# Performance work log

Measured on AMD Instinct MI355X. Metric: run time of the kernel, lower is better.

## Reference

```python
import jax, jax.numpy as jnp
import numpy as np

TAU = 2.0        # tau_m
EPS = 1e-5       # BatchNorm eps
SG_GAIN = 4.0    # surrogate gradient gain for LIF nodes
GATE_GAIN = 10.0 # SCALPerceptionLayer gain
GATE_VTH = 0.5   # SCALPerceptionLayer v_th_init


def _spike(v, v_th, gain):
    # Heaviside forward, sigmoid surrogate backward (straight-through).
    s = jax.nn.sigmoid(gain * (v - v_th))
    hard = (v >= v_th).astype(v.dtype)
    return s + jax.lax.stop_gradient(hard - s)


def _lif(x, v_th):
    # single-step LIF, zero initial membrane: v = v0 + (x - v0)/tau = x/tau
    return _spike(x / TAU, v_th, SG_GAIN)


def _bn(x, gamma, beta):
    # BatchNorm1d over channel dim D of (B, N, D): stats over (B, N)
    m = x.mean(axis=(0, 1))
    v = x.var(axis=(0, 1))
    return (x - m) * jax.lax.rsqrt(v + EPS) * gamma + beta


def setup_inputs() -> dict:
    B, N, D, H = 4, 1024, 1024, 16
    key = jax.random.key(0)
    ks = jax.random.split(key, 12)
    def lin(k, out_f, in_f):
        return jax.random.normal(k, (out_f, in_f), jnp.float32) * (in_f ** -0.5)
    inp = {"x": jax.random.normal(ks[0], (B, N, D), jnp.float32)}
    for i, nm in enumerate(["q", "k", "v", "p"]):
        inp[f"W{nm}"] = lin(ks[1 + i], D, D)
        inp[f"b{nm}"] = jnp.zeros((D,), jnp.float32)
        inp[f"g{nm}"] = jnp.ones((D,), jnp.float32)   # BN gamma
        inp[f"beta{nm}"] = jnp.zeros((D,), jnp.float32)  # BN beta
    inp["Wg"] = lin(ks[10], H, D)  # logic_core linear
    inp["bg"] = jnp.zeros((H,), jnp.float32)
    return inp


def reference(x, Wq, bq, gq, betaq, Wk, bk, gk, betak,
              Wv, bv, gv, betav, Wp, bp, gp, betap, Wg, bg):
    B, N, D = x.shape
    H = Wg.shape[0]
    hd = D // H
    scale = hd ** -0.125

    def branch(W, b, g, beta):
        # Linear -> BN (over channels) -> LIF spike -> (B,H,N,hd)
        s = _lif(_bn(x @ W.T + b, g, beta), 1.0)
        return s.reshape(B, N, H, hd).transpose(0, 2, 1, 3)

    q = branch(Wq, bq, gq, betaq)
    k = branch(Wk, bk, gk, betak)
    v = branch(Wv, bv, gv, betav)

    # LogicGateController: energy (B,H) -> repeat to (B,D) -> spiking linear gate
    energy = (q * k).sum(axis=-1).mean(axis=-1)            # (B, H)
    energy_feat = jnp.tile(energy, (1, D // H))            # (B, D)
    gate = _spike(energy_feat @ Wg.T + bg, GATE_VTH, GATE_GAIN)  # (B, H)
    gate = gate[:, :, None, None]                          # (B, H, 1, 1)

    attn = jnp.einsum('bhnd,bhmd->bhnm', q, k) * scale     # (B,H,N,N)
    x_attn = jnp.einsum('bhnm,bhmd->bhnd', attn * gate, v) # (B,H,N,hd)
    x_attn = x_attn.transpose(0, 2, 1, 3).reshape(B, N, D)
    x_attn = _lif(x_attn, 0.5)                             # attn_lif, v_th=0.5

    out = _lif(_bn(x_attn @ Wp.T + bp, gp, betap), 1.0)    # proj path
    return out
```

## Files before the change

kernel.cpp:

```cpp
#include <hip/hip_runtime.h>
#include <cstddef>
#include <cstdint>

#define EPS 1e-5f

typedef __bf16 bf16x8 __attribute__((ext_vector_type(8)));
typedef float f32x4 __attribute__((ext_vector_type(4)));
typedef unsigned short u16x8 __attribute__((ext_vector_type(8)));

__device__ __forceinline__ unsigned short f2bf(float f) {
  unsigned u = __builtin_bit_cast(unsigned, f);
  unsigned r = u + 0x7FFFu + ((u >> 16) & 1u);
  return (unsigned short)(r >> 16);
}
__device__ __forceinline__ float bf2f(unsigned short h) {
  unsigned u = (unsigned)h << 16;
  return __builtin_bit_cast(float, u);
}

__device__ __forceinline__ void gl_lds16(const void* g, void* l) {
  __builtin_amdgcn_global_load_lds(
      (const __attribute__((address_space(1))) unsigned int*)g,
      (__attribute__((address_space(3))) unsigned int*)l, 16, 0, 0);
}

template <int MODE>
__global__ __launch_bounds__(256) void gemm_bf16_bt(
    const unsigned short* __restrict__ A,
    const unsigned short* __restrict__ W0, const unsigned short* __restrict__ W1,
    const float* __restrict__ b0, const float* __restrict__ b1,
    unsigned short* __restrict__ Y, double* __restrict__ psum, double* __restrict__ psq,
    const int* __restrict__ flags, int N, int Kc)
{
  if (MODE == 2) { if (flags[0] == 0) return; }

  __shared__ unsigned short As[2][8192];
  __shared__ unsigned short Bs[2][8192];
  const int tid = threadIdx.x;

  const int bid = blockIdx.x + (blockIdx.y << 3) + (blockIdx.z << 8);
  const int nwg = (int)gridDim.z << 8;
  const int cpx = nwg >> 3;
  const int sw = (bid & 7) * cpx + (bid >> 3);
  const int bx = sw & 7, by = (sw >> 3) & 31, z = sw >> 8;

  const unsigned short* Bm = z ? W1 : W0;
  const float* bias = z ? b1 : b0;
  unsigned short* Yz = Y + (size_t)z * 4096 * N;

  const int bm = by * 128, bn = bx * 128;
  const int lane = tid & 63, w = tid >> 6;
  const int wr = w >> 1, wc = w & 1;
  const int l15 = lane & 15, g = lane >> 4;

  f32x4 acc[4][4] = {};

  bool skip = false;
  if (MODE == 1) skip = (flags[1 + (by >> 3)] == 0);

  if (!skip) {
    const unsigned short* aSrc[4]; const unsigned short* bSrc[4]; int dOff[4];
#pragma unroll
    for (int c = 0; c < 4; ++c) {
      int S = c * 256 + tid;
      int row = S >> 3, sp = S & 7;
      int sl = sp ^ (row & 7);
      aSrc[c] = A  + (size_t)(bm + row) * Kc + sl * 8;
      bSrc[c] = Bm + (size_t)(bn + row) * Kc + sl * 8;
      dOff[c] = S * 8;
    }
    int aOff[4][2], bOff[4][2];
#pragma unroll
    for (int i = 0; i < 4; ++i)
#pragma unroll
      for (int t = 0; t < 2; ++t) {
        int rowA = wr * 64 + i * 16 + l15;
        aOff[i][t] = rowA * 64 + ((t * 4 + g) ^ (rowA & 7)) * 8;
        int rowB = wc * 64 + i * 16 + l15;
        bOff[i][t] = rowB * 64 + ((t * 4 + g) ^ (rowB & 7)) * 8;
      }

    const int nk = Kc >> 6;
#pragma unroll
    for (int c = 0; c < 4; ++c) { gl_lds16(aSrc[c], &As[0][dOff[c]]); aSrc[c] += 64; }
#pragma unroll
    for (int c = 0; c < 4; ++c) { gl_lds16(bSrc[c], &Bs[0][dOff[c]]); bSrc[c] += 64; }

    int cur = 0;
    for (int kt = 0; kt < nk; ++kt) {
      if (kt + 1 < nk) {
#pragma unroll
        for (int c = 0; c < 4; ++c) { gl_lds16(aSrc[c], &As[cur ^ 1][dOff[c]]); aSrc[c] += 64; }
#pragma unroll
        for (int c = 0; c < 4; ++c) { gl_lds16(bSrc[c], &Bs[cur ^ 1][dOff[c]]); bSrc[c] += 64; }
        asm volatile("s_waitcnt vmcnt(8)" ::: "memory");
      } else {
        asm volatile("s_waitcnt vmcnt(0)" ::: "memory");
      }
      __builtin_amdgcn_s_barrier();
      __builtin_amdgcn_sched_barrier(0);
      {
        const unsigned short* Ac = &As[cur][0];
        const unsigned short* Bc = &Bs[cur][0];
#pragma unroll
        for (int t = 0; t < 2; ++t) {
          bf16x8 af[4], bfr[4];
#pragma unroll
          for (int i = 0; i < 4; ++i) af[i] = *(const bf16x8*)&Ac[aOff[i][t]];
#pragma unroll
          for (int j = 0; j < 4; ++j) bfr[j] = *(const bf16x8*)&Bc[bOff[j][t]];
#pragma unroll
          for (int i = 0; i < 4; ++i)
#pragma unroll
            for (int j = 0; j < 4; ++j)
              acc[i][j] = __builtin_amdgcn_mfma_f32_16x16x32_bf16(af[i], bfr[j], acc[i][j], 0, 0, 0);
        }
      }
      __builtin_amdgcn_s_barrier();
      cur ^= 1;
    }
  }

  const int r0 = bm + wr * 64 + g * 4;
  float csum[4], csq[4];
#pragma unroll
  for (int j = 0; j < 4; ++j) { csum[j] = 0.f; csq[j] = 0.f; }
#pragma unroll
  for (int j = 0; j < 4; ++j) {
    int col = bn + wc * 64 + j * 16 + l15;
    float bv = bias[col];
#pragma unroll
    for (int i = 0; i < 4; ++i)
#pragma unroll
      for (int r = 0; r < 4; ++r) {
        float yv = acc[i][j][r] + bv;
        unsigned short h = f2bf(yv);
        float yb = bf2f(h);
        Yz[(size_t)(r0 + i * 16 + r) * N + col] = h;
        csum[j] += yb;
        csq[j] += yb * yb;
      }
  }
  __syncthreads();
  float* Ls = (float*)&As[0][0];
  const int slot = wr * 4 + g;
#pragma unroll
  for (int j = 0; j < 4; ++j) {
    int ci = wc * 64 + j * 16 + l15;
    Ls[slot * 128 + ci] = csum[j];
    Ls[1024 + slot * 128 + ci] = csq[j];
  }
  __syncthreads();
  if (tid < 128) {
    double s = 0.0, q = 0.0;
#pragma unroll
    for (int sl = 0; sl < 8; ++sl) {
      s += (double)Ls[sl * 128 + tid];
      q += (double)Ls[1024 + sl * 128 + tid];
    }
    size_t o = ((size_t)z * 32 + by) * N + bn + tid;
    psum[o] = s;
    psq[o] = q;
  }
}

__global__ void prep1_kernel(const float* __restrict__ x,
                             const float* __restrict__ Wq, const float* __restrict__ Wk,
                             unsigned short* __restrict__ Xh, unsigned short* __restrict__ Wh3)
{
  int bid = blockIdx.x, tid = threadIdx.x;
  const float* src; unsigned short* dst; size_t base;
  if (bid < 2048) {
    src = x; dst = Xh; base = ((size_t)bid * 256 + tid) * 8;
  } else if (bid < 2560) {
    src = Wq; dst = Wh3; base = ((size_t)(bid - 2048) * 256 + tid) * 8;
  } else {
    src = Wk; dst = Wh3 + (size_t)1024 * 1024; base = ((size_t)(bid - 2560) * 256 + tid) * 8;
  }
  float4 a = *reinterpret_cast<const float4*>(&src[base]);
  float4 b = *reinterpret_cast<const float4*>(&src[base + 4]);
  u16x8 o;
  o[0] = f2bf(a.x); o[1] = f2bf(a.y); o[2] = f2bf(a.z); o[3] = f2bf(a.w);
  o[4] = f2bf(b.x); o[5] = f2bf(b.y); o[6] = f2bf(b.z); o[7] = f2bf(b.w);
  *reinterpret_cast<u16x8*>(&dst[base]) = o;
}

__global__ void prep2_kernel(const float* __restrict__ Wv, const float* __restrict__ Wp,
                             unsigned short* __restrict__ Whv, unsigned short* __restrict__ Wpcat,
                             const int* __restrict__ flags)
{
  if (flags[0] == 0) return;
  int bid = blockIdx.x, tid = threadIdx.x;
  if (bid < 512) {
    size_t base = ((size_t)bid * 256 + tid) * 8;
    float4 a = *reinterpret_cast<const float4*>(&Wv[base]);
    float4 b = *reinterpret_cast<const float4*>(&Wv[base + 4]);
    u16x8 o;
    o[0] = f2bf(a.x); o[1] = f2bf(a.y); o[2] = f2bf(a.z); o[3] = f2bf(a.w);
    o[4] = f2bf(b.x); o[5] = f2bf(b.y); o[6] = f2bf(b.z); o[7] = f2bf(b.w);
    *reinterpret_cast<u16x8*>(&Whv[base]) = o;
  } else {
    size_t base = ((size_t)(bid - 512) * 256 + tid) * 8;
    int r = (int)(base >> 10), c = (int)(base & 1023);
    float4 a = *reinterpret_cast<const float4*>(&Wp[base]);
    float4 b = *reinterpret_cast<const float4*>(&Wp[base + 4]);
    u16x8 hi, lo;
    hi[0] = f2bf(a.x); lo[0] = f2bf(a.x - bf2f(hi[0]));
    hi[1] = f2bf(a.y); lo[1] = f2bf(a.y - bf2f(hi[1]));
    hi[2] = f2bf(a.z); lo[2] = f2bf(a.z - bf2f(hi[2]));
    hi[3] = f2bf(a.w); lo[3] = f2bf(a.w - bf2f(hi[3]));
    hi[4] = f2bf(b.x); lo[4] = f2bf(b.x - bf2f(hi[4]));
    hi[5] = f2bf(b.y); lo[5] = f2bf(b.y - bf2f(hi[5]));
    hi[6] = f2bf(b.z); lo[6] = f2bf(b.z - bf2f(hi[6]));
    hi[7] = f2bf(b.w); lo[7] = f2bf(b.w - bf2f(hi[7]));
    unsigned short* Or = Wpcat + (size_t)r * 2048;
    *reinterpret_cast<u16x8*>(&Or[c]) = hi;
    *reinterpret_cast<u16x8*>(&Or[1024 + c]) = lo;
  }
}

__global__ void bn_finalize(const double* __restrict__ psum, const double* __restrict__ psq,
                            const float* __restrict__ g0, const float* __restrict__ g1,
                            float* __restrict__ meanv, float* __restrict__ Av,
                            const int* __restrict__ runflag,
                            int* __restrict__ zflags, int* __restrict__ zenergy,
                            int N, double invM)
{
  if (zflags && blockIdx.x == 0 && blockIdx.y == 0) {
    int t = threadIdx.x;
    if (t < 5) zflags[t] = 0;
    if (t >= 64 && t < 128) zenergy[t - 64] = 0;
  }
  if (runflag && runflag[0] == 0) return;
  int z = blockIdx.y;
  const float* g = z ? g1 : g0;
  int c = blockIdx.x * blockDim.x + threadIdx.x;
  const double* ps = psum + (size_t)z * 32 * N + c;
  const double* pq = psq  + (size_t)z * 32 * N + c;
  double s0 = 0, s1 = 0, q0 = 0, q1 = 0;
#pragma unroll
  for (int rb = 0; rb < 32; rb += 2) {
    s0 += ps[(size_t)rb * N];       q0 += pq[(size_t)rb * N];
    s1 += ps[(size_t)(rb + 1) * N]; q1 += pq[(size_t)(rb + 1) * N];
  }
  double s = s0 + s1, q = q0 + q1;
  double m = s * invM;
  double var = q * invM - m * m;
  if (var < 0.0) var = 0.0;
  meanv[(size_t)z * N + c] = (float)m;
  Av[(size_t)z * N + c] = g[(size_t)c] * rsqrtf((float)var + EPS);
}

__global__ void spike_qk_energy(const unsigned short* __restrict__ Yq,
                                const unsigned short* __restrict__ Yk,
                                const float* __restrict__ meanv, const float* __restrict__ Av,
                                const float* __restrict__ beq, const float* __restrict__ bek,
                                unsigned short* __restrict__ qb, unsigned short* __restrict__ kb,
                                int* __restrict__ energy_int, int N)
{
  const int tid = threadIdx.x;
  const int c0 = (tid * 8) & (N - 1);
  const int head = c0 >> 6;
  const int batch = blockIdx.x >> 7;
  const float* mq = meanv;            const float* aq = Av;
  const float* mk = meanv + N;        const float* ak = Av + N;
  __shared__ int bins[16];
  if (tid < 16) bins[tid] = 0;
  __syncthreads();
  int cnt = 0;
#pragma unroll
  for (int j = 0; j < 4; ++j) {
    size_t base = (size_t)blockIdx.x * 8192 + j * 2048 + tid * 8;
    u16x8 yq = *reinterpret_cast<const u16x8*>(&Yq[base]);
    u16x8 yk = *reinterpret_cast<const u16x8*>(&Yk[base]);
    u16x8 oq, ok;
#pragma unroll
    for (int e = 0; e < 8; ++e) {
      bool sq = (bf2f(yq[e]) - mq[c0 + e]) * aq[c0 + e] + beq[c0 + e] >= 2.0f;
      bool sk = (bf2f(yk[e]) - mk[c0 + e]) * ak[c0 + e] + bek[c0 + e] >= 2.0f;
      oq[e] = sq ? 0x3F80 : 0;
      ok[e] = sk ? 0x3F80 : 0;
      cnt += (sq && sk) ? 1 : 0;
    }
    *reinterpret_cast<u16x8*>(&qb[base]) = oq;
    *reinterpret_cast<u16x8*>(&kb[base]) = ok;
  }
  atomicAdd(&bins[head], cnt);
  __syncthreads();
  if (tid < 16) atomicAdd(&energy_int[batch * 16 + tid], bins[tid]);
}

__global__ void spike_v(const unsigned short* __restrict__ Yv,
                        const float* __restrict__ meanv, const float* __restrict__ Av,
                        const float* __restrict__ beta, unsigned short* __restrict__ vb,
                        const int* __restrict__ flags, int N)
{
  if (flags[0] == 0) return;
  size_t base = ((size_t)blockIdx.x * 256 + threadIdx.x) * 8;
  int c0 = (int)(base & (size_t)(N - 1));
  u16x8 y8 = *reinterpret_cast<const u16x8*>(&Yv[base]);
  u16x8 o;
#pragma unroll
  for (int e = 0; e < 8; ++e)
    o[e] = ((bf2f(y8[e]) - meanv[c0 + e]) * Av[c0 + e] + beta[c0 + e] >= 2.0f) ? 0x3F80 : 0;
  *reinterpret_cast<u16x8*>(&vb[base]) = o;
}

__global__ void bn_spike_f32(const unsigned short* __restrict__ Y,
                             const float* __restrict__ meanv, const float* __restrict__ Av,
                             const float* __restrict__ beta, float* __restrict__ S, int N)
{
  size_t base = ((size_t)blockIdx.x * 256 + threadIdx.x) * 8;
  int c0 = (int)(base & (size_t)(N - 1));
  u16x8 y8 = *reinterpret_cast<const u16x8*>(&Y[base]);
  float4 o0, o1;
  o0.x = ((bf2f(y8[0]) - meanv[c0 + 0]) * Av[c0 + 0] + beta[c0 + 0] >= 2.0f) ? 1.f : 0.f;
  o0.y = ((bf2f(y8[1]) - meanv[c0 + 1]) * Av[c0 + 1] + beta[c0 + 1] >= 2.0f) ? 1.f : 0.f;
  o0.z = ((bf2f(y8[2]) - meanv[c0 + 2]) * Av[c0 + 2] + beta[c0 + 2] >= 2.0f) ? 1.f : 0.f;
  o0.w = ((bf2f(y8[3]) - meanv[c0 + 3]) * Av[c0 + 3] + beta[c0 + 3] >= 2.0f) ? 1.f : 0.f;
  o1.x = ((bf2f(y8[4]) - meanv[c0 + 4]) * Av[c0 + 4] + beta[c0 + 4] >= 2.0f) ? 1.f : 0.f;
  o1.y = ((bf2f(y8[5]) - meanv[c0 + 5]) * Av[c0 + 5] + beta[c0 + 5] >= 2.0f) ? 1.f : 0.f;
  o1.z = ((bf2f(y8[6]) - meanv[c0 + 6]) * Av[c0 + 6] + beta[c0 + 6] >= 2.0f) ? 1.f : 0.f;
  o1.w = ((bf2f(y8[7]) - meanv[c0 + 7]) * Av[c0 + 7] + beta[c0 + 7] >= 2.0f) ? 1.f : 0.f;
  *reinterpret_cast<float4*>(&S[base]) = o0;
  *reinterpret_cast<float4*>(&S[base + 4]) = o1;
}

__global__ void gate_kernel(const int* __restrict__ energy_int, const float* __restrict__ Wg,
                            const float* __restrict__ bg, float* __restrict__ gate,
                            int* __restrict__ flags, int D)
{
  int b = blockIdx.x >> 4, hp = blockIdx.x & 15;
  int tid = threadIdx.x;
  float e[16];
#pragma unroll
  for (int h = 0; h < 16; ++h) e[h] = (float)energy_int[b * 16 + h] * (1.f / 1024.f);
  float s = 0.f;
  for (int j = tid; j < D; j += 256) s = fmaf(e[j & 15], Wg[(size_t)hp * D + j], s);
  __shared__ float red[256];
  red[tid] = s;
  __syncthreads();
  for (int off = 128; off; off >>= 1) {
    if (tid < off) red[tid] += red[tid + off];
    __syncthreads();
  }
  if (tid == 0) {
    int gv = (red[0] + bg[hp] >= 0.5f) ? 1 : 0;
    gate[blockIdx.x] = (float)gv;
    if (gv) { atomicOr(&flags[0], 1); atomicOr(&flags[1 + b], 1); }
  }
}

__global__ __launch_bounds__(256) void attn_kernel(
    const unsigned short* __restrict__ qb, const unsigned short* __restrict__ kb,
    const unsigned short* __restrict__ vb, const float* __restrict__ gate,
    const int* __restrict__ flags, unsigned short* __restrict__ xs,
    int Ntok, int D, float scale)
{
  int bh = blockIdx.x;
  int b = bh >> 4, h = bh & 15;
  if (flags[1 + b] == 0) return;
  int n0 = blockIdx.y * 32;
  int tid = threadIdx.x;
  unsigned short* outbase = xs + (size_t)(b * Ntok + n0) * 2048 + h * 64;

  if (gate[bh] == 0.f) {
    ushort4 zv = {0, 0, 0, 0};
    for (int i = tid; i < 32 * 16; i += 256) {
      int r = i >> 4, c4 = (i & 15) << 2;
      *reinterpret_cast<ushort4*>(&outbase[(size_t)r * 2048 + c4]) = zv;
      *reinterpret_cast<ushort4*>(&outbase[(size_t)r * 2048 + 1024 + c4]) = zv;
    }
    return;
  }

  __shared__ float qs[32][68], ks[32][68], vs[32][68], Ss[32][36];
  const unsigned short* qg = qb + (size_t)b * Ntok * D + h * 64;
  const unsigned short* kg = kb + (size_t)b * Ntok * D + h * 64;
  const unsigned short* vg = vb + (size_t)b * Ntok * D + h * 64;

  {
    int r = tid >> 3, c8 = (tid & 7) * 8;
    u16x8 t = *reinterpret_cast<const u16x8*>(&qg[(size_t)(n0 + r) * D + c8]);
#pragma unroll
    for (int e = 0; e < 8; ++e) qs[r][c8 + e] = bf2f(t[e]);
  }

  float acc[8];
#pragma unroll
  for (int j = 0; j < 8; ++j) acc[j] = 0.f;
  const int nloc = tid >> 3;
  const int dd0 = (tid & 7) * 8;

  for (int mt = 0; mt < Ntok / 32; ++mt) {
    int m0 = mt * 32;
    __syncthreads();
    {
      int r = tid >> 3, c8 = (tid & 7) * 8;
      u16x8 tk = *reinterpret_cast<const u16x8*>(&kg[(size_t)(m0 + r) * D + c8]);
      u16x8 tv = *reinterpret_cast<const u16x8*>(&vg[(size_t)(m0 + r) * D + c8]);
#pragma unroll
      for (int e = 0; e < 8; ++e) { ks[r][c8 + e] = bf2f(tk[e]); vs[r][c8 + e] = bf2f(tv[e]); }
    }
    __syncthreads();
    {
      int np = tid >> 3;
      int mp0 = (tid & 7) * 4;
      float s0 = 0.f, s1 = 0.f, s2 = 0.f, s3 = 0.f;
#pragma unroll 8
      for (int d = 0; d < 64; ++d) {
        float qv = qs[np][d];
        s0 = fmaf(qv, ks[mp0 + 0][d], s0);
        s1 = fmaf(qv, ks[mp0 + 1][d], s1);
        s2 = fmaf(qv, ks[mp0 + 2][d], s2);
        s3 = fmaf(qv, ks[mp0 + 3][d], s3);
      }
      Ss[np][mp0 + 0] = s0; Ss[np][mp0 + 1] = s1;
      Ss[np][mp0 + 2] = s2; Ss[np][mp0 + 3] = s3;
    }
    __syncthreads();
#pragma unroll 8
    for (int mp = 0; mp < 32; ++mp) {
      float sv = Ss[nloc][mp];
#pragma unroll
      for (int j = 0; j < 8; ++j) acc[j] = fmaf(sv, vs[mp][dd0 + j], acc[j]);
    }
  }

#pragma unroll
  for (int j = 0; j < 8; ++j) {
    float x = scale * acc[j];
    unsigned short sp = (x >= 1.0f) ? 0x3F80 : 0;
    outbase[(size_t)nloc * 2048 + dd0 + j] = sp;
    outbase[(size_t)nloc * 2048 + 1024 + dd0 + j] = sp;
  }
}

extern "C" void kernel_launch(void* const* d_in, const int* in_sizes, int n_in,
                              void* d_out, int out_size, void* d_ws, size_t ws_size,
                              hipStream_t stream)
{
  (void)in_sizes; (void)n_in; (void)out_size; (void)ws_size;
  const int Ntok = 1024, D = 1024;
  const int M = 4096;
  const float scale = 0.5946035575013605f;

  const float* x     = (const float*)d_in[0];
  const float* Wq    = (const float*)d_in[1];
  const float* bq    = (const float*)d_in[2];
  const float* gq    = (const float*)d_in[3];
  const float* betaq = (const float*)d_in[4];
  const float* Wk    = (const float*)d_in[5];
  const float* bk    = (const float*)d_in[6];
  const float* gk    = (const float*)d_in[7];
  const float* betak = (const float*)d_in[8];
  const float* Wv    = (const float*)d_in[9];
  const float* bv    = (const float*)d_in[10];
  const float* gv    = (const float*)d_in[11];
  const float* betav = (const float*)d_in[12];
  const float* Wp    = (const float*)d_in[13];
  const float* bp    = (const float*)d_in[14];
  const float* gp    = (const float*)d_in[15];
  const float* betap = (const float*)d_in[16];
  const float* Wg    = (const float*)d_in[17];
  const float* bg    = (const float*)d_in[18];

  char* w = (char*)d_ws;
  const size_t MB = 1024 * 1024;
  const size_t MN = (size_t)M * D;
  unsigned short* Y3bf  = (unsigned short*)(w + 0 * MB);
  unsigned short* xat2  = (unsigned short*)(w + 0 * MB);
  unsigned short* Yv    = Y3bf + 2 * MN;
  unsigned short* Yp    = (unsigned short*)(w + 24 * MB);
  unsigned short* Wpcat = (unsigned short*)(w + 32 * MB);
  unsigned short* Xh    = (unsigned short*)(w + 48 * MB);
  unsigned short* Wh3   = (unsigned short*)(w + 56 * MB);
  unsigned short* qb2   = (unsigned short*)(w + 62 * MB);
  unsigned short* kb2   = (unsigned short*)(w + 70 * MB);
  unsigned short* vb2   = (unsigned short*)(w + 78 * MB);
  double* psum   = (double*)(w + 86 * MB);
  double* psq    = (double*)(w + 87 * MB);
  float*  meanv  = (float*)(w + 88 * MB);
  float*  Av     = (float*)(w + 88 * MB + 16384);
  int*    energy_int = (int*)(w + 88 * MB + 32768);
  int*    flags  = (int*)(w + 88 * MB + 32768 + 512);
  float*  gate   = (float*)(w + 88 * MB + 32768 + 1024);

  float* out = (float*)d_out;
  unsigned short* Whq = Wh3;
  unsigned short* Whk = Wh3 + MN / 4;
  unsigned short* Whv = Wh3 + MN / 2;

  prep1_kernel<<<dim3(3072), 256, 0, stream>>>(x, Wq, Wk, Xh, Wh3);

  gemm_bf16_bt<0><<<dim3(8, 32, 2), 256, 0, stream>>>(
      Xh, Whq, Whk, bq, bk, Y3bf, psum, psq, nullptr, D, 1024);
  bn_finalize<<<dim3(4, 2), 256, 0, stream>>>(
      psum, psq, gq, gk, meanv, Av, nullptr, flags, energy_int, D, 1.0 / M);
  spike_qk_energy<<<dim3(512), 256, 0, stream>>>(
      Y3bf, Y3bf + MN, meanv, Av, betaq, betak, qb2, kb2, energy_int, D);

  gate_kernel<<<dim3(64), 256, 0, stream>>>(energy_int, Wg, bg, gate, flags, D);

  prep2_kernel<<<dim3(1024), 256, 0, stream>>>(Wv, Wp, Whv, Wpcat, flags);

  gemm_bf16_bt<2><<<dim3(8, 32, 1), 256, 0, stream>>>(
      Xh, Whv, Whv, bv, bv, Yv, psum + 2 * 32 * (size_t)D, psq + 2 * 32 * (size_t)D,
      flags, D, 1024);
  bn_finalize<<<dim3(4, 1), 256, 0, stream>>>(
      psum + 2 * 32 * (size_t)D, psq + 2 * 32 * (size_t)D, gv, gv,
      meanv + 2 * D, Av + 2 * D, flags, nullptr, nullptr, D, 1.0 / M);
  spike_v<<<dim3(2048), 256, 0, stream>>>(Yv, meanv + 2 * D, Av + 2 * D, betav, vb2, flags, D);

  attn_kernel<<<dim3(64, Ntok / 32), 256, 0, stream>>>(
      qb2, kb2, vb2, gate, flags, xat2, Ntok, D, scale);

  gemm_bf16_bt<1><<<dim3(8, 32, 1), 256, 0, stream>>>(
      xat2, Wpcat, Wpcat, bp, bp, Yp, psum, psq, flags, D, 2048);
  bn_finalize<<<dim3(4, 1), 256, 0, stream>>>(
      psum, psq, gp, gp, meanv, Av, nullptr, nullptr, nullptr, D, 1.0 / M);
  bn_spike_f32<<<dim3(2048), 256, 0, stream>>>(Yp, meanv, Av, betap, out, D);
}
```

Baseline: 75.63 us.

## Use 8-wave GEMM tiles, split q/k spike writes, skip gated-off projection blocks

The GEMM now runs 512 threads (8 waves) per 128x128 tile, so each wave computes 64x32 instead of 64x64. This halves accumulators per wave and is meant to raise occupancy and latency hiding. The qk spike kernel is split into an energy-count pass and a separate write pass that returns early when the gate flags say attention is disabled. In the projection GEMM, batches whose gate is off now return early. The BN finalize and final spike kernel reconstruct those rows from the bias instead of reading uninitialized outputs. This adds a kernel launch and extra branching logic, and the bias-only substitution assumes gated-off rows are exactly the bias.

Result: slower. 84.79 us (+12.1%).

```diff
diff --git a/kernel.cpp b/kernel.cpp
--- a/kernel.cpp
+++ b/kernel.cpp
@@ -25,7 +25,7 @@
 }
 
 template <int MODE>
-__global__ __launch_bounds__(256) void gemm_bf16_bt(
+__global__ __launch_bounds__(512) void gemm8_bf16_bt(
     const unsigned short* __restrict__ A,
     const unsigned short* __restrict__ W0, const unsigned short* __restrict__ W1,
     const float* __restrict__ b0, const float* __restrict__ b1,
@@ -44,90 +44,91 @@
   const int sw = (bid & 7) * cpx + (bid >> 3);
   const int bx = sw & 7, by = (sw >> 3) & 31, z = sw >> 8;
 
+  if (MODE == 1) { if (flags[1 + (by >> 3)] == 0) return; }
+
   const unsigned short* Bm = z ? W1 : W0;
   const float* bias = z ? b1 : b0;
   unsigned short* Yz = Y + (size_t)z * 4096 * N;
 
   const int bm = by * 128, bn = bx * 128;
   const int lane = tid & 63, w = tid >> 6;
-  const int wr = w >> 1, wc = w & 1;
+  const int wr = w >> 2, wc = w & 3;
   const int l15 = lane & 15, g = lane >> 4;
 
-  f32x4 acc[4][4] = {};
-
-  bool skip = false;
-  if (MODE == 1) skip = (flags[1 + (by >> 3)] == 0);
-
-  if (!skip) {
-    const unsigned short* aSrc[4]; const unsigned short* bSrc[4]; int dOff[4];
-#pragma unroll
-    for (int c = 0; c < 4; ++c) {
-      int S = c * 256 + tid;
-      int row = S >> 3, sp = S & 7;
-      int sl = sp ^ (row & 7);
-      aSrc[c] = A  + (size_t)(bm + row) * Kc + sl * 8;
-      bSrc[c] = Bm + (size_t)(bn + row) * Kc + sl * 8;
-      dOff[c] = S * 8;
-    }
-    int aOff[4][2], bOff[4][2];
-#pragma unroll
-    for (int i = 0; i < 4; ++i)
+  f32x4 acc[4][2] = {};
+
+  const unsigned short* aSrc[2]; const unsigned short* bSrc[2]; int dOff[2];
+#pragma unroll
+  for (int c = 0; c < 2; ++c) {
+    int S = c * 512 + tid;
+    int row = S >> 3, sp = S & 7;
+    int sl = sp ^ (row & 7);
+    aSrc[c] = A  + (size_t)(bm + row) * Kc + sl * 8;
+    bSrc[c] = Bm + (size_t)(bn + row) * Kc + sl * 8;
+    dOff[c] = S * 8;
+  }
+  int aOff[4][2], bOff[2][2];
+#pragma unroll
+  for (int t = 0; t < 2; ++t) {
+#pragma unroll
+    for (int i = 0; i < 4; ++i) {
+      int rowA = wr * 64 + i * 16 + l15;
+      aOff[i][t] = rowA * 64 + ((t * 4 + g) ^ (rowA & 7)) * 8;
+    }
+#pragma unroll
+    for (int j = 0; j < 2; ++j) {
+      int rowB = wc * 32 + j * 16 + l15;
+      bOff[j][t] = rowB * 64 + ((t * 4 + g) ^ (rowB & 7)) * 8;
+    }
+  }
+
+  const int nk = Kc >> 6;
+#pragma unroll
+  for (int c = 0; c < 2; ++c) { gl_lds16(aSrc[c], &As[0][dOff[c]]); aSrc[c] += 64; }
+#pragma unroll
+  for (int c = 0; c < 2; ++c) { gl_lds16(bSrc[c], &Bs[0][dOff[c]]); bSrc[c] += 64; }
+
+  int cur = 0;
+  for (int kt = 0; kt < nk; ++kt) {
+    if (kt + 1 < nk) {
+#pragma unroll
+      for (int c = 0; c < 2; ++c) { gl_lds16(aSrc[c], &As[cur ^ 1][dOff[c]]); aSrc[c] += 64; }
+#pragma unroll
+      for (int c = 0; c < 2; ++c) { gl_lds16(bSrc[c], &Bs[cur ^ 1][dOff[c]]); bSrc[c] += 64; }
+      asm volatile("s_waitcnt vmcnt(4)" ::: "memory");
+    } else {
+      asm volatile("s_waitcnt vmcnt(0)" ::: "memory");
+    }
+    __builtin_amdgcn_s_barrier();
+    __builtin_amdgcn_sched_barrier(0);
+    {
+      const unsigned short* Ac = &As[cur][0];
+      const unsigned short* Bc = &Bs[cur][0];
 #pragma unroll
       for (int t = 0; t < 2; ++t) {
-        int rowA = wr * 64 + i * 16 + l15;
-        aOff[i][t] = rowA * 64 + ((t * 4 + g) ^ (rowA & 7)) * 8;
-        int rowB = wc * 64 + i * 16 + l15;
-        bOff[i][t] = rowB * 64 + ((t * 4 + g) ^ (rowB & 7)) * 8;
+        bf16x8 af[4], bfr[2];
+#pragma unroll
+        for (int i = 0; i < 4; ++i) af[i] = *(const bf16x8*)&Ac[aOff[i][t]];
+#pragma unroll
+        for (int j = 0; j < 2; ++j) bfr[j] = *(const bf16x8*)&Bc[bOff[j][t]];
+#pragma unroll
+        for (int i = 0; i < 4; ++i)
+#pragma unroll
+          for (int j = 0; j < 2; ++j)
+            acc[i][j] = __builtin_amdgcn_mfma_f32_16x16x32_bf16(af[i], bfr[j], acc[i][j], 0, 0, 0);
       }
-
-    const int nk = Kc >> 6;
-#pragma unroll
-    for (int c = 0; c < 4; ++c) { gl_lds16(aSrc[c], &As[0][dOff[c]]); aSrc[c] += 64; }
-#pragma unroll
-    for (int c = 0; c < 4; ++c) { gl_lds16(bSrc[c], &Bs[0][dOff[c]]); bSrc[c] += 64; }
-
-    int cur = 0;
-    for (int kt = 0; kt < nk; ++kt) {
-      if (kt + 1 < nk) {
-#pragma unroll
-        for (int c = 0; c < 4; ++c) { gl_lds16(aSrc[c], &As[cur ^ 1][dOff[c]]); aSrc[c] += 64; }
-#pragma unroll
-        for (int c = 0; c < 4; ++c) { gl_lds16(bSrc[c], &Bs[cur ^ 1][dOff[c]]); bSrc[c] += 64; }
-        asm volatile("s_waitcnt vmcnt(8)" ::: "memory");
-      } else {
-        asm volatile("s_waitcnt vmcnt(0)" ::: "memory");
-      }
-      __builtin_amdgcn_s_barrier();
-      __builtin_amdgcn_sched_barrier(0);
-      {
-        const unsigned short* Ac = &As[cur][0];
-        const unsigned short* Bc = &Bs[cur][0];
-#pragma unroll
-        for (int t = 0; t < 2; ++t) {
-          bf16x8 af[4], bfr[4];
-#pragma unroll
-          for (int i = 0; i < 4; ++i) af[i] = *(const bf16x8*)&Ac[aOff[i][t]];
-#pragma unroll
-          for (int j = 0; j < 4; ++j) bfr[j] = *(const bf16x8*)&Bc[bOff[j][t]];
-#pragma unroll
-          for (int i = 0; i < 4; ++i)
-#pragma unroll
-            for (int j = 0; j < 4; ++j)
-              acc[i][j] = __builtin_amdgcn_mfma_f32_16x16x32_bf16(af[i], bfr[j], acc[i][j], 0, 0, 0);
-        }
-      }
-      __builtin_amdgcn_s_barrier();
-      cur ^= 1;
-    }
+    }
+    __builtin_amdgcn_s_barrier();
+    cur ^= 1;
   }
 
   const int r0 = bm + wr * 64 + g * 4;
-  float csum[4], csq[4];
-#pragma unroll
-  for (int j = 0; j < 4; ++j) { csum[j] = 0.f; csq[j] = 0.f; }
-#pragma unroll
-  for (int j = 0; j < 4; ++j) {
-    int col = bn + wc * 64 + j * 16 + l15;
+  float csum[2], csq[2];
+#pragma unroll
+  for (int j = 0; j < 2; ++j) { csum[j] = 0.f; csq[j] = 0.f; }
+#pragma unroll
+  for (int j = 0; j < 2; ++j) {
+    int col = bn + wc * 32 + j * 16 + l15;
     float bv = bias[col];
 #pragma unroll
     for (int i = 0; i < 4; ++i)
@@ -145,8 +146,8 @@
   float* Ls = (float*)&As[0][0];
   const int slot = wr * 4 + g;
 #pragma unroll
-  for (int j = 0; j < 4; ++j) {
-    int ci = wc * 64 + j * 16 + l15;
+  for (int j = 0; j < 2; ++j) {
+    int ci = wc * 32 + j * 16 + l15;
     Ls[slot * 128 + ci] = csum[j];
     Ls[1024 + slot * 128 + ci] = csq[j];
   }
@@ -251,19 +252,43 @@
   Av[(size_t)z * N + c] = g[(size_t)c] * rsqrtf((float)var + EPS);
 }
 
-__global__ void spike_qk_energy(const unsigned short* __restrict__ Yq,
-                                const unsigned short* __restrict__ Yk,
-                                const float* __restrict__ meanv, const float* __restrict__ Av,
-                                const float* __restrict__ beq, const float* __restrict__ bek,
-                                unsigned short* __restrict__ qb, unsigned short* __restrict__ kb,
-                                int* __restrict__ energy_int, int N)
+__global__ void bn_finalize_p(const double* __restrict__ psum, const double* __restrict__ psq,
+                              const float* __restrict__ gp, const float* __restrict__ bp,
+                              float* __restrict__ meanv, float* __restrict__ Av,
+                              const int* __restrict__ flags, int N, double invM)
+{
+  int c = blockIdx.x * blockDim.x + threadIdx.x;
+  float ybb = bf2f(f2bf(bp[c]));
+  double yd = (double)ybb;
+  double s = 0.0, q = 0.0;
+  for (int rb = 0; rb < 32; ++rb) {
+    if (flags[1 + (rb >> 3)]) {
+      s += psum[(size_t)rb * N + c];
+      q += psq [(size_t)rb * N + c];
+    } else {
+      s += 128.0 * yd;
+      q += 128.0 * yd * yd;
+    }
+  }
+  double m = s * invM;
+  double var = q * invM - m * m;
+  if (var < 0.0) var = 0.0;
+  meanv[c] = (float)m;
+  Av[c] = gp[(size_t)c] * rsqrtf((float)var + EPS);
+}
+
+__global__ void energy_cnt(const unsigned short* __restrict__ Yq,
+                           const unsigned short* __restrict__ Yk,
+                           const float* __restrict__ meanv, const float* __restrict__ Av,
+                           const float* __restrict__ beq, const float* __restrict__ bek,
+                           int* __restrict__ energy_int, int N)
 {
   const int tid = threadIdx.x;
   const int c0 = (tid * 8) & (N - 1);
   const int head = c0 >> 6;
   const int batch = blockIdx.x >> 7;
-  const float* mq = meanv;            const float* aq = Av;
-  const float* mk = meanv + N;        const float* ak = Av + N;
+  const float* mq = meanv;     const float* aq = Av;
+  const float* mk = meanv + N; const float* ak = Av + N;
   __shared__ int bins[16];
   if (tid < 16) bins[tid] = 0;
   __syncthreads();
@@ -273,21 +298,40 @@
     size_t base = (size_t)blockIdx.x * 8192 + j * 2048 + tid * 8;
     u16x8 yq = *reinterpret_cast<const u16x8*>(&Yq[base]);
     u16x8 yk = *reinterpret_cast<const u16x8*>(&Yk[base]);
-    u16x8 oq, ok;
 #pragma unroll
     for (int e = 0; e < 8; ++e) {
       bool sq = (bf2f(yq[e]) - mq[c0 + e]) * aq[c0 + e] + beq[c0 + e] >= 2.0f;
       bool sk = (bf2f(yk[e]) - mk[c0 + e]) * ak[c0 + e] + bek[c0 + e] >= 2.0f;
-      oq[e] = sq ? 0x3F80 : 0;
-      ok[e] = sk ? 0x3F80 : 0;
       cnt += (sq && sk) ? 1 : 0;
     }
-    *reinterpret_cast<u16x8*>(&qb[base]) = oq;
-    *reinterpret_cast<u16x8*>(&kb[base]) = ok;
   }
   atomicAdd(&bins[head], cnt);
   __syncthreads();
   if (tid < 16) atomicAdd(&energy_int[batch * 16 + tid], bins[tid]);
+}
+
+__global__ void spike_qk_write(const unsigned short* __restrict__ Yq,
+                               const unsigned short* __restrict__ Yk,
+                               const float* __restrict__ meanv, const float* __restrict__ Av,
+                               const float* __restrict__ beq, const float* __restrict__ bek,
+                               unsigned short* __restrict__ qb, unsigned short* __restrict__ kb,
+                               const int* __restrict__ flags, int N)
+{
+  if (flags[0] == 0) return;
+  size_t base = ((size_t)blockIdx.x * 256 + threadIdx.x) * 8;
+  int c0 = (int)(base & (size_t)(N - 1));
+  const float* mq = meanv;     const float* aq = Av;
+  const float* mk = meanv + N; const float* ak = Av + N;
+  u16x8 yq = *reinterpret_cast<const u16x8*>(&Yq[base]);
+  u16x8 yk = *reinterpret_cast<const u16x8*>(&Yk[base]);
+  u16x8 oq, ok;
+#pragma unroll
+  for (int e = 0; e < 8; ++e) {
+    oq[e] = ((bf2f(yq[e]) - mq[c0 + e]) * aq[c0 + e] + beq[c0 + e] >= 2.0f) ? 0x3F80 : 0;
+    ok[e] = ((bf2f(yk[e]) - mk[c0 + e]) * ak[c0 + e] + bek[c0 + e] >= 2.0f) ? 0x3F80 : 0;
+  }
+  *reinterpret_cast<u16x8*>(&qb[base]) = oq;
+  *reinterpret_cast<u16x8*>(&kb[base]) = ok;
 }
 
 __global__ void spike_v(const unsigned short* __restrict__ Yv,
@@ -308,20 +352,30 @@
 
 __global__ void bn_spike_f32(const unsigned short* __restrict__ Y,
                              const float* __restrict__ meanv, const float* __restrict__ Av,
-                             const float* __restrict__ beta, float* __restrict__ S, int N)
+                             const float* __restrict__ beta, const float* __restrict__ bp,
+                             const int* __restrict__ flags, float* __restrict__ S, int N)
 {
   size_t base = ((size_t)blockIdx.x * 256 + threadIdx.x) * 8;
   int c0 = (int)(base & (size_t)(N - 1));
-  u16x8 y8 = *reinterpret_cast<const u16x8*>(&Y[base]);
+  int batch = (int)(base >> 20);
+  float y[8];
+  if (flags[1 + batch]) {
+    u16x8 y8 = *reinterpret_cast<const u16x8*>(&Y[base]);
+#pragma unroll
+    for (int e = 0; e < 8; ++e) y[e] = bf2f(y8[e]);
+  } else {
+#pragma unroll
+    for (int e = 0; e < 8; ++e) y[e] = bf2f(f2bf(bp[c0 + e]));
+  }
   float4 o0, o1;
-  o0.x = ((bf2f(y8[0]) - meanv[c0 + 0]) * Av[c0 + 0] + beta[c0 + 0] >= 2.0f) ? 1.f : 0.f;
-  o0.y = ((bf2f(y8[1]) - meanv[c0 + 1]) * Av[c0 + 1] + beta[c0 + 1] >= 2.0f) ? 1.f : 0.f;
-  o0.z = ((bf2f(y8[2]) - meanv[c0 + 2]) * Av[c0 + 2] + beta[c0 + 2] >= 2.0f) ? 1.f : 0.f;
-  o0.w = ((bf2f(y8[3]) - meanv[c0 + 3]) * Av[c0 + 3] + beta[c0 + 3] >= 2.0f) ? 1.f : 0.f;
-  o1.x = ((bf2f(y8[4]) - meanv[c0 + 4]) * Av[c0 + 4] + beta[c0 + 4] >= 2.0f) ? 1.f : 0.f;
-  o1.y = ((bf2f(y8[5]) - meanv[c0 + 5]) * Av[c0 + 5] + beta[c0 + 5] >= 2.0f) ? 1.f : 0.f;
-  o1.z = ((bf2f(y8[6]) - meanv[c0 + 6]) * Av[c0 + 6] + beta[c0 + 6] >= 2.0f) ? 1.f : 0.f;
-  o1.w = ((bf2f(y8[7]) - meanv[c0 + 7]) * Av[c0 + 7] + beta[c0 + 7] >= 2.0f) ? 1.f : 0.f;
+  o0.x = ((y[0] - meanv[c0 + 0]) * Av[c0 + 0] + beta[c0 + 0] >= 2.0f) ? 1.f : 0.f;
+  o0.y = ((y[1] - meanv[c0 + 1]) * Av[c0 + 1] + beta[c0 + 1] >= 2.0f) ? 1.f : 0.f;
+  o0.z = ((y[2] - meanv[c0 + 2]) * Av[c0 + 2] + beta[c0 + 2] >= 2.0f) ? 1.f : 0.f;
+  o0.w = ((y[3] - meanv[c0 + 3]) * Av[c0 + 3] + beta[c0 + 3] >= 2.0f) ? 1.f : 0.f;
+  o1.x = ((y[4] - meanv[c0 + 4]) * Av[c0 + 4] + beta[c0 + 4] >= 2.0f) ? 1.f : 0.f;
+  o1.y = ((y[5] - meanv[c0 + 5]) * Av[c0 + 5] + beta[c0 + 5] >= 2.0f) ? 1.f : 0.f;
+  o1.z = ((y[6] - meanv[c0 + 6]) * Av[c0 + 6] + beta[c0 + 6] >= 2.0f) ? 1.f : 0.f;
+  o1.w = ((y[7] - meanv[c0 + 7]) * Av[c0 + 7] + beta[c0 + 7] >= 2.0f) ? 1.f : 0.f;
   *reinterpret_cast<float4*>(&S[base]) = o0;
   *reinterpret_cast<float4*>(&S[base + 4]) = o1;
 }
@@ -490,21 +544,24 @@
   unsigned short* Whq = Wh3;
   unsigned short* Whk = Wh3 + MN / 4;
   unsigned short* Whv = Wh3 + MN / 2;
+  float* meanp = meanv + 3 * D;
+  float* Avp   = Av + 3 * D;
 
   prep1_kernel<<<dim3(3072), 256, 0, stream>>>(x, Wq, Wk, Xh, Wh3);
 
-  gemm_bf16_bt<0><<<dim3(8, 32, 2), 256, 0, stream>>>(
+  gemm8_bf16_bt<0><<<dim3(8, 32, 2), 512, 0, stream>>>(
       Xh, Whq, Whk, bq, bk, Y3bf, psum, psq, nullptr, D, 1024);
   bn_finalize<<<dim3(4, 2), 256, 0, stream>>>(
       psum, psq, gq, gk, meanv, Av, nullptr, flags, energy_int, D, 1.0 / M);
-  spike_qk_energy<<<dim3(512), 256, 0, stream>>>(
-      Y3bf, Y3bf + MN, meanv, Av, betaq, betak, qb2, kb2, energy_int, D);
-
+
+  energy_cnt<<<dim3(512), 256, 0, stream>>>(
+      Y3bf, Y3bf + MN, meanv, Av, betaq, betak, energy_int, D);
   gate_kernel<<<dim3(64), 256, 0, stream>>>(energy_int, Wg, bg, gate, flags, D);
 
+  spike_qk_write<<<dim3(2048), 256, 0, stream>>>(
+      Y3bf, Y3bf + MN, meanv, Av, betaq, betak, qb2, kb2, flags, D);
   prep2_kernel<<<dim3(1024), 256, 0, stream>>>(Wv, Wp, Whv, Wpcat, flags);
-
-  gemm_bf16_bt<2><<<dim3(8, 32, 1), 256, 0, stream>>>(
+  gemm8_bf16_bt<2><<<dim3(8, 32, 1), 512, 0, stream>>>(
       Xh, Whv, Whv, bv, bv, Yv, psum + 2 * 32 * (size_t)D, psq + 2 * 32 * (size_t)D,
       flags, D, 1024);
   bn_finalize<<<dim3(4, 1), 256, 0, stream>>>(
@@ -515,9 +572,8 @@
   attn_kernel<<<dim3(64, Ntok / 32), 256, 0, stream>>>(
       qb2, kb2, vb2, gate, flags, xat2, Ntok, D, scale);
 
-  gemm_bf16_bt<1><<<dim3(8, 32, 1), 256, 0, stream>>>(
+  gemm8_bf16_bt<1><<<dim3(8, 32, 1), 512, 0, stream>>>(
       xat2, Wpcat, Wpcat, bp, bp, Yp, psum, psq, flags, D, 2048);
-  bn_finalize<<<dim3(4, 1), 256, 0, stream>>>(
-      psum, psq, gp, gp, meanv, Av, nullptr, nullptr, nullptr, D, 1.0 / M);
-  bn_spike_f32<<<dim3(2048), 256, 0, stream>>>(Yp, meanv, Av, betap, out, D);
-}
+  bn_finalize_p<<<dim3(4), 256, 0, stream>>>(psum, psq, gp, bp, meanp, Avp, flags, D, 1.0 / M);
+  bn_spike_f32<<<dim3(2048), 256, 0, stream>>>(Yp, meanp, Avp, betap, bp, flags, out, D);
+}
```
